# Kernel optimization log

Hardware: AMD Instinct MI355X
Metric: run time of the kernel (lower is better)

The kernel has to match this reference:

```python
import jax, jax.numpy as jnp
import numpy as np

B, T, D = 4, 4096, 2048
K = 1024
H, KVH, HD = 16, 4, 128
FF = 8192
EPS = 1e-6


def _rmsnorm(x, w):
    v = jnp.mean(x * x, axis=-1, keepdims=True)
    return x * jax.lax.rsqrt(v + EPS) * w


def _rotate_half(x):
    x1, x2 = jnp.split(x, 2, axis=-1)
    return jnp.concatenate([-x2, x1], axis=-1)


def setup_inputs() -> dict:
    key = jax.random.key(0)
    ks = jax.random.split(key, 16)
    hidden_states = jax.random.normal(ks[0], (B, T, D), dtype=jnp.float32)
    # unique sorted indices per sequence (top-k selection without duplicates)
    scores = jax.random.uniform(ks[1], (B, T))
    topk_indices = jnp.sort(jax.lax.top_k(scores, K)[1], axis=-1).astype(jnp.int64)
    gating_scores = jax.random.uniform(ks[2], (B, K), dtype=jnp.float32)
    # rotary embeddings over the full sequence [B, T, HD]
    inv = 1.0 / (10000.0 ** (jnp.arange(0, HD, 2, dtype=jnp.float32) / HD))
    ang = jnp.arange(T, dtype=jnp.float32)[:, None] * inv[None, :]  # [T, HD/2]
    emb = jnp.concatenate([ang, ang], axis=-1)
    cos = jnp.broadcast_to(jnp.cos(emb)[None], (B, T, HD)).astype(jnp.float32)
    sin = jnp.broadcast_to(jnp.sin(emb)[None], (B, T, HD)).astype(jnp.float32)
    s = 0.02
    params = dict(
        Wq=jax.random.normal(ks[3], (D, H * HD)) * s,
        bq=jnp.zeros((H * HD,)),
        Wk=jax.random.normal(ks[4], (D, KVH * HD)) * s,
        bk=jnp.zeros((KVH * HD,)),
        Wv=jax.random.normal(ks[5], (D, KVH * HD)) * s,
        bv=jnp.zeros((KVH * HD,)),
        Wo=jax.random.normal(ks[6], (H * HD, D)) * s,
        w_gate=jax.random.normal(ks[7], (D, FF)) * s,
        w_up=jax.random.normal(ks[8], (D, FF)) * s,
        w_down=jax.random.normal(ks[9], (FF, D)) * s,
        ln1_w=jnp.ones((D,)),
        ln2_w=jnp.ones((D,)),
    )
    return dict(hidden_states=hidden_states, topk_indices=topk_indices,
                gating_scores=gating_scores, cos=cos, sin=sin, **params)


def _decoder_layer(x, cos_s, sin_s, Wq, bq, Wk, bk, Wv, bv, Wo,
                   w_gate, w_up, w_down, ln1_w, ln2_w):
    # x: [B, K, D]; cos_s/sin_s: [B, K, HD]
    res = x
    h = _rmsnorm(x, ln1_w)
    q = (h @ Wq + bq).reshape(B, K, H, HD)
    k = (h @ Wk + bk).reshape(B, K, KVH, HD)
    v = (h @ Wv + bv).reshape(B, K, KVH, HD)
    c = cos_s[:, :, None, :]
    s = sin_s[:, :, None, :]
    q = q * c + _rotate_half(q) * s
    k = k * c + _rotate_half(k) * s
    # GQA: repeat kv heads
    k = jnp.repeat(k, H // KVH, axis=2)
    v = jnp.repeat(v, H // KVH, axis=2)
    scores = jnp.einsum('bqhd,bkhd->bhqk', q, k) / np.sqrt(HD)
    causal = jnp.tril(jnp.ones((K, K), dtype=bool))
    scores = jnp.where(causal[None, None], scores, jnp.finfo(scores.dtype).min)
    attn = jax.nn.softmax(scores, axis=-1)
    out = jnp.einsum('bhqk,bkhd->bqhd', attn, v).reshape(B, K, H * HD)
    x = res + out @ Wo
    # MLP (SwiGLU)
    res = x
    h = _rmsnorm(x, ln2_w)
    x = res + (jax.nn.silu(h @ w_gate) * (h @ w_up)) @ w_down
    return x


def reference(hidden_states, topk_indices, gating_scores, cos, sin,
              Wq, bq, Wk, bk, Wv, bv, Wo, w_gate, w_up, w_down, ln1_w, ln2_w):
    idx = topk_indices[:, :, None]  # [B, K, 1]
    selected = jnp.take_along_axis(hidden_states, idx, axis=1)  # [B, K, D]
    cos_s = jnp.take_along_axis(cos, idx, axis=1)
    sin_s = jnp.take_along_axis(sin, idx, axis=1)
    processed = _decoder_layer(selected, cos_s, sin_s, Wq, bq, Wk, bk, Wv, bv,
                               Wo, w_gate, w_up, w_down, ln1_w, ln2_w)
    # soft gating: selected + gate * (processed - selected)
    updated = selected + (processed - selected) * gating_scores[:, :, None]
    b_idx = jnp.arange(B)[:, None]
    final = hidden_states.at[b_idx, topk_indices].set(updated)
    return final
```

## Files before the change

kernel.cpp:

```cpp
#include <hip/hip_runtime.h>
#include <stdint.h>

typedef __bf16 bf16;
typedef __attribute__((ext_vector_type(8))) __bf16 bf16x8;
typedef __attribute__((ext_vector_type(4))) float f32x4;

namespace {

constexpr int cB = 4, cT = 4096, cD = 2048, cK = 1024, cH = 16, cKVH = 4, cHD = 128, cFF = 8192;
constexpr int cM = cB * cK;
constexpr int QKVW = cH * cHD + 2 * cKVH * cHD;

__device__ __forceinline__ void load_lds16(const void* g, void* l) {
  __builtin_amdgcn_global_load_lds((const __attribute__((address_space(1))) void*)g,
                                   (__attribute__((address_space(3))) void*)l, 16, 0, 0);
}

template <int N>
__device__ __forceinline__ void waitcnt_vm() {
  if constexpr (N == 0) asm volatile("s_waitcnt vmcnt(0)" ::: "memory");
  else if constexpr (N == 2) asm volatile("s_waitcnt vmcnt(2)" ::: "memory");
  else if constexpr (N == 3) asm volatile("s_waitcnt vmcnt(3)" ::: "memory");
  else if constexpr (N == 4) asm volatile("s_waitcnt vmcnt(4)" ::: "memory");
  else if constexpr (N == 6) asm volatile("s_waitcnt vmcnt(6)" ::: "memory");
  else if constexpr (N == 8) asm volatile("s_waitcnt vmcnt(8)" ::: "memory");
  else static_assert(N == 0, "unsupported vmcnt literal");
}

template <int OP>
__device__ __forceinline__ float blk_reduce(float v) {
  __shared__ float sm[5];
  const int tid = threadIdx.x, lane = tid & 63, wid = tid >> 6;
#pragma unroll
  for (int o = 32; o; o >>= 1) {
    float o2 = __shfl_down(v, o, 64);
    v = OP ? fmaxf(v, o2) : v + o2;
  }
  if (lane == 0) sm[wid] = v;
  __syncthreads();
  if (tid == 0) {
    float r = sm[0];
#pragma unroll
    for (int i = 1; i < 4; ++i) r = OP ? fmaxf(r, sm[i]) : r + sm[i];
    sm[4] = r;
  }
  __syncthreads();
  float r = sm[4];
  __syncthreads();
  return r;
}

template <int BN, int WM, int WN, int RING, int UNROLL, class Epi>
__global__ __launch_bounds__(512, 2)
void gemm256(const bf16* __restrict__ A, int lda,
             const bf16* __restrict__ Bm, int ldb,
             int Kd, int GM, Epi epi) {
  constexpr int BM = 256;
  constexpr int FM = BM / WM / 16;
  constexpr int FN = BN / WN / 16;
  constexpr int ACALLS = 2;
  constexpr int BCALLS = BN / 128;
  constexpr int L = ACALLS + BCALLS;
  constexpr int D = RING - 1;
  constexpr int SLOTA = BM * 64;
  constexpr int SLOTB = BN * 64;
  constexpr int SLOT = SLOTA + SLOTB;
  __shared__ __align__(16) char lds[RING * SLOT];

  const int tid = threadIdx.x;
  const int lane = tid & 63;
  const int wid = tid >> 6;
  const int l15 = lane & 15, lq = lane >> 4;
  const int wr = wid / WN, wc = wid % WN;

  const int nwg = gridDim.x;
  const int xcd = blockIdx.x & 7, loc = blockIdx.x >> 3;
  const int wg = xcd * (nwg >> 3) + loc;
  const int GN = nwg / GM;
  const int per = 8 * GN;
  const int g = wg / per, r = wg % per;
  const int bm = g * 8 + (r & 7);
  const int bn = r >> 3;

  const bf16* Abase = A + (int64_t)bm * BM * lda;
  const bf16* Bbase = Bm + (int64_t)bn * BN * ldb;

  const bf16* srcA[ACALLS];
  int dstA[ACALLS];
#pragma unroll
  for (int c2 = 0; c2 < ACALLS; ++c2) {
    const int chunk = c2 * 512 + tid;
    const int row = chunk >> 2, pc = chunk & 3;
    const int lc = pc ^ ((row >> 1) & 3);
    srcA[c2] = Abase + (int64_t)row * lda + lc * 8;
    dstA[c2] = chunk * 16;
  }
  const bf16* srcB[BCALLS];
  int dstB[BCALLS];
#pragma unroll
  for (int c2 = 0; c2 < BCALLS; ++c2) {
    const int chunk = c2 * 512 + tid;
    const int row = chunk >> 2, pc = chunk & 3;
    const int lc = pc ^ ((row >> 1) & 3);
    srcB[c2] = Bbase + (int64_t)row * ldb + lc * 8;
    dstB[c2] = chunk * 16;
  }

  int offA[FM], offB[FN];
#pragma unroll
  for (int m = 0; m < FM; ++m) {
    const int row = wr * (BM / WM) + m * 16 + l15;
    offA[m] = row * 64 + (lq ^ ((row >> 1) & 3)) * 16;
  }
#pragma unroll
  for (int n = 0; n < FN; ++n) {
    const int row = wc * (BN / WN) + n * 16 + l15;
    offB[n] = SLOTA + row * 64 + (lq ^ ((row >> 1) & 3)) * 16;
  }

  const int KT = Kd >> 5;
  auto stage = [&](int t) {
    char* sb = lds + (size_t)(t % RING) * SLOT;
#pragma unroll
    for (int c2 = 0; c2 < ACALLS; ++c2)
      load_lds16(srcA[c2] + t * 32, sb + dstA[c2]);
#pragma unroll
    for (int c2 = 0; c2 < BCALLS; ++c2)
      load_lds16(srcB[c2] + t * 32, sb + SLOTA + dstB[c2]);
  };
  auto compute = [&](int t, f32x4 (&acc)[FM][FN]) {
    const char* sb = lds + (size_t)(t % RING) * SLOT;
    bf16x8 av[FM], bv[FN];
#pragma unroll
    for (int m = 0; m < FM; ++m) av[m] = *(const bf16x8*)(sb + offA[m]);
#pragma unroll
    for (int n = 0; n < FN; ++n) bv[n] = *(const bf16x8*)(sb + offB[n]);
    __builtin_amdgcn_s_setprio(1);
#pragma unroll
    for (int m = 0; m < FM; ++m)
#pragma unroll
      for (int n = 0; n < FN; ++n)
        acc[m][n] = __builtin_amdgcn_mfma_f32_16x16x32_bf16(av[m], bv[n], acc[m][n], 0, 0, 0);
    __builtin_amdgcn_s_setprio(0);
  };

  f32x4 acc[FM][FN] = {};

  if constexpr (UNROLL == 1) {
#pragma unroll
    for (int i = 0; i < D; ++i) stage(i);
    waitcnt_vm<(D - 1) * L>();
    __builtin_amdgcn_s_barrier();
    __builtin_amdgcn_sched_barrier(0);
    for (int t = 0; t < KT - D; ++t) {
      stage(t + D);
      compute(t, acc);
      waitcnt_vm<(D - 1) * L>();
      __builtin_amdgcn_s_barrier();
      __builtin_amdgcn_sched_barrier(0);
    }
    waitcnt_vm<0>();
    __builtin_amdgcn_s_barrier();
    for (int t = KT - D; t < KT; ++t) compute(t, acc);
  } else {
    static_assert(RING == 5 && UNROLL == 2, "pair mode is RING=5");
#pragma unroll
    for (int i = 0; i < 3; ++i) stage(i);
    waitcnt_vm<L>();
    __builtin_amdgcn_s_barrier();
    __builtin_amdgcn_sched_barrier(0);
    int t = 0;
    for (; t <= KT - 6; t += 2) {
      stage(t + 3);
      stage(t + 4);
      compute(t, acc);
      compute(t + 1, acc);
      waitcnt_vm<L>();
      __builtin_amdgcn_s_barrier();
      __builtin_amdgcn_sched_barrier(0);
    }
    stage(KT - 1);
    waitcnt_vm<0>();
    __builtin_amdgcn_s_barrier();
    compute(KT - 4, acc);
    compute(KT - 3, acc);
    compute(KT - 2, acc);
    compute(KT - 1, acc);
  }

#pragma unroll
  for (int m = 0; m < FM; ++m) {
    const int r0 = bm * BM + wr * (BM / WM) + m * 16 + lq * 4;
#pragma unroll
    for (int n = 0; n < FN; ++n) {
      const int c1 = bn * BN + wc * (BN / WN) + n * 16 + l15;
#pragma unroll
      for (int j = 0; j < 4; ++j) epi(r0 + j, c1, acc[m][n][j]);
    }
  }
}

__global__ __launch_bounds__(512, 2)
void gemm_gateup8(const bf16* __restrict__ A, const bf16* __restrict__ Bgu,
                  bf16* __restrict__ act) {
  constexpr int QSZ = 64 * 128;
  __shared__ __align__(16) char lds[2 * 8 * QSZ];

  const int tid = threadIdx.x, lane = tid & 63;
  const int wid = tid >> 6;
  const int l15 = lane & 15, lq = lane >> 4;
  const int wr = wid >> 2, wc = wid & 3;

  const int nwg = gridDim.x;
  const int xcd = blockIdx.x & 7, loc = blockIdx.x >> 3;
  const int wg = xcd * (nwg >> 3) + loc;
  const int GM = 16, GN = nwg / GM;
  const int per = 8 * GN;
  const int g = wg / per, r = wg % per;
  const int bm = g * 8 + (r & 7);
  const int bn = r >> 3;

  const bf16* Abase = A + (int64_t)bm * 256 * cD;
  const bf16* Bbase = Bgu + (int64_t)bn * 256 * cD;

  const int srow = tid >> 3, spc = tid & 7;
  const int slc = spc ^ (srow & 7);
  const int sdst = tid * 16;
  const bf16* qsrc[8];
#pragma unroll
  for (int q = 0; q < 4; ++q) qsrc[q] = Abase + (int64_t)(q * 64 + srow) * cD + slc * 8;
#pragma unroll
  for (int q = 0; q < 4; ++q) qsrc[4 + q] = Bbase + (int64_t)(q * 64 + srow) * cD + slc * 8;

  auto stageQ = [&](int buf, int q, int kt) {
    load_lds16(qsrc[q] + kt * 64, lds + (size_t)(buf * 8 + q) * QSZ + sdst);
  };

  f32x4 acc[8][4] = {};
  bf16x8 af[4][2], bfr[2][2];

  auto ldA = [&](int buf, int qr) {
    const char* qb = lds + (size_t)(buf * 8 + wr * 2 + qr) * QSZ;
#pragma unroll
    for (int mq = 0; mq < 4; ++mq) {
      const int rr = mq * 16 + l15;
#pragma unroll
      for (int ks = 0; ks < 2; ++ks)
        af[mq][ks] = *(const bf16x8*)(qb + rr * 128 + (((ks * 4 + lq) ^ (rr & 7)) * 16));
    }
  };
  auto ldB = [&](int buf, int qc) {
    const char* qb = lds + (size_t)(buf * 8 + 4 + wc) * QSZ;
#pragma unroll
    for (int nq = 0; nq < 2; ++nq) {
      const int rr = qc * 32 + nq * 16 + l15;
#pragma unroll
      for (int ks = 0; ks < 2; ++ks)
        bfr[nq][ks] = *(const bf16x8*)(qb + rr * 128 + (((ks * 4 + lq) ^ (rr & 7)) * 16));
    }
  };
  auto mfma16 = [&](int qr, int qc) {
    __builtin_amdgcn_s_setprio(1);
#pragma unroll
    for (int ks = 0; ks < 2; ++ks)
#pragma unroll
      for (int mq = 0; mq < 4; ++mq)
#pragma unroll
        for (int nq = 0; nq < 2; ++nq)
          acc[qr * 4 + mq][qc * 2 + nq] = __builtin_amdgcn_mfma_f32_16x16x32_bf16(
              af[mq][ks], bfr[nq][ks], acc[qr * 4 + mq][qc * 2 + nq], 0, 0, 0);
    __builtin_amdgcn_s_setprio(0);
  };

  const int KT = cD >> 6;

  stageQ(0, 4, 0); stageQ(0, 5, 0);
  stageQ(0, 6, 0); stageQ(0, 7, 0);
  stageQ(0, 0, 0); stageQ(0, 2, 0);
  stageQ(0, 1, 0); stageQ(0, 3, 0);
  waitcnt_vm<2>();
  __builtin_amdgcn_s_barrier();

  for (int t = 0; t < KT; ++t) {
    const int buf = t & 1, nb = buf ^ 1;
    const bool more = (t + 1 < KT);
    ldA(buf, 0);
    ldB(buf, 0);
    if (more) { stageQ(nb, 4, t + 1); stageQ(nb, 5, t + 1); }
    __builtin_amdgcn_s_barrier();
    mfma16(0, 0);
    __builtin_amdgcn_s_barrier();
    ldB(buf, 1);
    if (more) { stageQ(nb, 6, t + 1); stageQ(nb, 7, t + 1); }
    __builtin_amdgcn_s_barrier();
    mfma16(0, 1);
    if (more) waitcnt_vm<4>();
    else      waitcnt_vm<0>();
    __builtin_amdgcn_s_barrier();
    ldA(buf, 1);
    if (more) { stageQ(nb, 0, t + 1); stageQ(nb, 2, t + 1); }
    __builtin_amdgcn_s_barrier();
    mfma16(1, 1);
    __builtin_amdgcn_s_barrier();
    ldB(buf, 0);
    if (more) { stageQ(nb, 1, t + 1); stageQ(nb, 3, t + 1); }
    __builtin_amdgcn_s_barrier();
    mfma16(1, 0);
    if (more) waitcnt_vm<2>();
    __builtin_amdgcn_s_barrier();
  }

#pragma unroll
  for (int m = 0; m < 8; ++m) {
    const int row = bm * 256 + wr * 128 + (m >> 2) * 64 + (m & 3) * 16 + lq * 4;
#pragma unroll
    for (int p = 0; p < 2; ++p) {
      const int col = bn * 128 + wc * 32 + p * 16 + l15;
#pragma unroll
      for (int j = 0; j < 4; ++j) {
        float gv = acc[m][2 * p][j];
        float s = gv / (1.f + __expf(-gv));
        act[(int64_t)(row + j) * cFF + col] = (bf16)(s * acc[m][2 * p + 1][j]);
      }
    }
  }
}

struct EpiQKV {
  bf16* out; const float* bias;
  __device__ void operator()(int r, int c, float v) const {
    out[(int64_t)r * QKVW + c] = (bf16)(v + bias[c]);
  }
};
struct EpiOProj {
  float* x; const float* hidden; const int* topk;
  __device__ void operator()(int r, int c, float v) const {
    int b = r >> 10;
    int t = topk[r];
    x[(int64_t)r * cD + c] = v + hidden[((int64_t)b * cT + t) * cD + c];
  }
};
struct EpiDown {
  float* out; const float* x; const float* hidden; const int* topk; const float* gating;
  __device__ void operator()(int r, int c, float v) const {
    int b = r >> 10;
    int t = topk[r];
    float x2 = v + x[(int64_t)r * cD + c];
    int64_t ho = ((int64_t)b * cT + t) * cD + c;
    float sel = hidden[ho];
    out[ho] = sel + (x2 - sel) * gating[r];
  }
};

__global__ __launch_bounds__(256, 2) void flash_attn(const bf16* __restrict__ qkv,
                                                     const bf16* __restrict__ vt,
                                                     bf16* __restrict__ outb) {
  constexpr int QB = 64, KVB = 128;
  __shared__ __align__(16) char lds[81920];
  char* sK = lds;
  char* sP = lds + 32768;
  char* sV = lds + 49152;

  const int xcdid = blockIdx.x & 7, locid = blockIdx.x >> 3;
  const int wg = xcdid * 128 + locid;
  const int qt = wg & 15, h = (wg >> 4) & 15, b = wg >> 8;
  const int kvh = h >> 2;
  const int qlo = qt * QB;
  const int tid = threadIdx.x, lane = tid & 63, wid = tid >> 6;
  const int l15 = lane & 15, lq = lane >> 4;
  const int wid16 = wid * 16;

  const bf16* qbase = qkv + (int64_t)(b * cK + qlo) * QKVW + h * cHD;
  const bf16* kbase = qkv + (int64_t)(b * cK) * QKVW + cH * cHD + kvh * cHD;
  const bf16* vtbase = vt + (int64_t)(b * cKVH + kvh) * cHD * cK;

#pragma unroll
  for (int c2 = 0; c2 < 4; ++c2) {
    int chunk = c2 * 256 + tid;
    int row = chunk >> 4, c16 = chunk & 15;
    load_lds16(qbase + (int64_t)row * QKVW + (c16 ^ (row & 15)) * 8, sK + chunk * 16);
  }
  __syncthreads();
  bf16x8 qf[4];
  {
    const int row = wid16 + l15;
#pragma unroll
    for (int kt = 0; kt < 4; ++kt)
      qf[kt] = *(const bf16x8*)(sK + row * 256 + (((kt * 4 + lq) ^ (row & 15)) * 16));
  }
  __syncthreads();

  f32x4 oacc[8] = {};
  float m_run[4], l_run[4];
#pragma unroll
  for (int j = 0; j < 4; ++j) { m_run[j] = -3.0e38f; l_run[j] = 0.f; }

  const int jmax = (qlo + QB - 1) >> 7;
  const float sl2e = 0.08838834764831845f * 1.44269504088896f;

  for (int jj = 0; jj <= jmax; ++jj) {
#pragma unroll
    for (int c2 = 0; c2 < 8; ++c2) {
      int chunk = c2 * 256 + tid;
      int row = chunk >> 4, c16 = chunk & 15;
      int cs = (c16 ^ (row & 15)) * 8;
      load_lds16(kbase + (int64_t)(jj * KVB + row) * QKVW + cs, sK + chunk * 16);
      load_lds16(vtbase + (int64_t)row * cK + jj * KVB + cs, sV + chunk * 16);
    }
    __syncthreads();

    f32x4 sacc[8] = {};
#pragma unroll
    for (int kt = 0; kt < 4; ++kt) {
      bf16x8 bv[8];
#pragma unroll
      for (int n = 0; n < 8; ++n) {
        int rk = n * 16 + l15;
        bv[n] = *(const bf16x8*)(sK + rk * 256 + (((kt * 4 + lq) ^ (rk & 15)) * 16));
      }
#pragma unroll
      for (int n = 0; n < 8; ++n)
        sacc[n] = __builtin_amdgcn_mfma_f32_16x16x32_bf16(qf[kt], bv[n], sacc[n], 0, 0, 0);
    }

    if (jj == jmax) {
#pragma unroll
      for (int n = 0; n < 8; ++n)
#pragma unroll
        for (int j = 0; j < 4; ++j) {
          int qrow = qlo + wid16 + lq * 4 + j;
          int kcol = jj * KVB + n * 16 + l15;
          if (kcol > qrow) sacc[n][j] = -3.0e38f;
        }
    }

#pragma unroll
    for (int j = 0; j < 4; ++j) {
      float mx = sacc[0][j];
#pragma unroll
      for (int n = 1; n < 8; ++n) mx = fmaxf(mx, sacc[n][j]);
#pragma unroll
      for (int off = 1; off < 16; off <<= 1) mx = fmaxf(mx, __shfl_xor(mx, off, 64));
      float mnew = fmaxf(m_run[j], mx);
      float corr = exp2f((m_run[j] - mnew) * sl2e);
      m_run[j] = mnew;
      float ps = 0.f;
#pragma unroll
      for (int n = 0; n < 8; ++n) {
        float p = exp2f((sacc[n][j] - mnew) * sl2e);
        sacc[n][j] = p;
        ps += p;
      }
#pragma unroll
      for (int off = 1; off < 16; off <<= 1) ps += __shfl_xor(ps, off, 64);
      l_run[j] = l_run[j] * corr + ps;
#pragma unroll
      for (int n = 0; n < 8; ++n) oacc[n][j] *= corr;
    }

#pragma unroll
    for (int n = 0; n < 8; ++n)
#pragma unroll
      for (int j = 0; j < 4; ++j) {
        int row = wid16 + lq * 4 + j;
        int col = n * 16 + l15;
        int c16 = (col >> 3) ^ (row & 15);
        *(bf16*)(sP + row * 256 + c16 * 16 + (col & 7) * 2) = (bf16)sacc[n][j];
      }
    __syncthreads();

#pragma unroll
    for (int kt = 0; kt < 4; ++kt) {
      const int prow = wid16 + l15;
      bf16x8 av = *(const bf16x8*)(sP + prow * 256 + (((kt * 4 + lq) ^ (prow & 15)) * 16));
      bf16x8 bv[8];
#pragma unroll
      for (int n = 0; n < 8; ++n) {
        int rd = n * 16 + l15;
        bv[n] = *(const bf16x8*)(sV + rd * 256 + (((kt * 4 + lq) ^ (rd & 15)) * 16));
      }
#pragma unroll
      for (int n = 0; n < 8; ++n)
        oacc[n] = __builtin_amdgcn_mfma_f32_16x16x32_bf16(av, bv[n], oacc[n], 0, 0, 0);
    }
    __syncthreads();
  }

#pragma unroll
  for (int j = 0; j < 4; ++j) {
    int row = qlo + wid16 + lq * 4 + j;
    float inv = 1.f / l_run[j];
#pragma unroll
    for (int n = 0; n < 8; ++n) {
      int col = h * cHD + n * 16 + l15;
      outb[((int64_t)b * cK + row) * cD + col] = (bf16)(oacc[n][j] * inv);
    }
  }
}

__global__ void copy_skip(const float4* __restrict__ s, float4* __restrict__ d,
                          const unsigned char* __restrict__ flags, int64_t n) {
  int64_t i = (int64_t)blockIdx.x * blockDim.x + threadIdx.x;
  const int64_t st = (int64_t)gridDim.x * blockDim.x;
  for (; i < n; i += st) {
    int row = (int)(i >> 9);
    if (!flags[row]) d[i] = s[i];
  }
}

__global__ void build_flags(const int* __restrict__ topk, unsigned char* __restrict__ flags) {
  int r = blockIdx.x * 256 + threadIdx.x;
  if (r < cM) flags[(r >> 10) * cT + topk[r]] = 1;
}

__global__ void wconv(const float* __restrict__ src, bf16* __restrict__ dst,
                      int R, int C, int coff, int ldd) {
  __shared__ float t[32][33];
  const int c0 = blockIdx.x * 32, r0 = blockIdx.y * 32;
  for (int rr = threadIdx.y; rr < 32; rr += 8)
    t[rr][threadIdx.x] = src[(int64_t)(r0 + rr) * C + c0 + threadIdx.x];
  __syncthreads();
  for (int rr = threadIdx.y; rr < 32; rr += 8)
    dst[(int64_t)(c0 + rr + coff) * ldd + r0 + threadIdx.x] = (bf16)t[threadIdx.x][rr];
}

__global__ void wconv_gu(const float* __restrict__ srcG, const float* __restrict__ srcU,
                         bf16* __restrict__ dst) {
  __shared__ float t[32][33];
  const float* src = blockIdx.z ? srcU : srcG;
  const int c0 = blockIdx.x * 32, r0 = blockIdx.y * 32;
  for (int rr = threadIdx.y; rr < 32; rr += 8)
    t[rr][threadIdx.x] = src[(int64_t)(r0 + rr) * cFF + c0 + threadIdx.x];
  __syncthreads();
  for (int rr = threadIdx.y; rr < 32; rr += 8) {
    int c = c0 + rr;
    int dr = ((c & ~15) << 1) | (blockIdx.z ? 16 : 0) | (c & 15);
    dst[(int64_t)dr * cD + r0 + threadIdx.x] = (bf16)t[threadIdx.x][rr];
  }
}

__global__ void biascat(const float* __restrict__ bq, const float* __restrict__ bk,
                        const float* __restrict__ bv, float* __restrict__ o) {
  int i = blockIdx.x * 256 + threadIdx.x;
  if (i < QKVW) o[i] = (i < 2048) ? bq[i] : (i < 2560 ? bk[i - 2048] : bv[i - 2560]);
}

__global__ void rmsnorm_rows(const float* __restrict__ base, const int* __restrict__ topk,
                             const float* __restrict__ w, bf16* __restrict__ out) {
  const int r = blockIdx.x;
  const float* src;
  if (topk) {
    int t = topk[r];
    src = base + ((int64_t)(r >> 10) * cT + t) * cD;
  } else {
    src = base + (int64_t)r * cD;
  }
  const int tid = threadIdx.x;
  const float4* s4 = (const float4*)src;
  float4 a = s4[tid * 2], b = s4[tid * 2 + 1];
  float ss = a.x * a.x + a.y * a.y + a.z * a.z + a.w * a.w +
             b.x * b.x + b.y * b.y + b.z * b.z + b.w * b.w;
  float tot = blk_reduce<0>(ss);
  float sc = rsqrtf(tot * (1.f / cD) + 1e-6f);
  bf16* o = out + (int64_t)r * cD;
  const int d0 = tid * 8;
  o[d0 + 0] = (bf16)(a.x * sc * w[d0 + 0]);
  o[d0 + 1] = (bf16)(a.y * sc * w[d0 + 1]);
  o[d0 + 2] = (bf16)(a.z * sc * w[d0 + 2]);
  o[d0 + 3] = (bf16)(a.w * sc * w[d0 + 3]);
  o[d0 + 4] = (bf16)(b.x * sc * w[d0 + 4]);
  o[d0 + 5] = (bf16)(b.y * sc * w[d0 + 5]);
  o[d0 + 6] = (bf16)(b.z * sc * w[d0 + 6]);
  o[d0 + 7] = (bf16)(b.w * sc * w[d0 + 7]);
}

__global__ void rope_kernel(bf16* __restrict__ qkv, const float* __restrict__ cosb,
                            const float* __restrict__ sinb, const int* __restrict__ topk) {
  const int r = blockIdx.x;
  const int b = r >> 10;
  const int t = topk[r];
  const float* cr = cosb + ((int64_t)b * cT + t) * cHD;
  const float* sr = sinb + ((int64_t)b * cT + t) * cHD;
  bf16* rowq = qkv + (int64_t)r * QKVW;
  for (int p = threadIdx.x; p < (cH + cKVH) * 64; p += 256) {
    int hh = p >> 6, d = p & 63;
    bf16* base = (hh < cH) ? (rowq + hh * cHD) : (rowq + cH * cHD + (hh - cH) * cHD);
    float x1 = (float)base[d], x2 = (float)base[d + 64];
    float c1 = cr[d], s1 = sr[d], c2 = cr[d + 64], s2 = sr[d + 64];
    base[d] = (bf16)(x1 * c1 - x2 * s1);
    base[d + 64] = (bf16)(x2 * c2 + x1 * s2);
  }
}

__global__ void vtrans(const bf16* __restrict__ qkv, bf16* __restrict__ Vt) {
  __shared__ bf16 t[32][33];
  const int bz = blockIdx.z, b = bz >> 2, kv = bz & 3;
  const int k0 = blockIdx.x * 32, d0 = blockIdx.y * 32;
  for (int rr = threadIdx.y; rr < 32; rr += 8)
    t[rr][threadIdx.x] =
        qkv[(int64_t)(b * cK + k0 + rr) * QKVW + cH * cHD + cKVH * cHD + kv * cHD + d0 + threadIdx.x];
  __syncthreads();
  for (int rr = threadIdx.y; rr < 32; rr += 8)
    Vt[((int64_t)(b * cKVH + kv) * cHD + d0 + rr) * cK + k0 + threadIdx.x] = t[threadIdx.x][rr];
}

}

extern "C" void kernel_launch(void* const* d_in, const int* in_sizes, int n_in,
                              void* d_out, int out_size, void* d_ws, size_t ws_size,
                              hipStream_t stream) {
  const float* hidden = (const float*)d_in[0];
  const int* topk = (const int*)d_in[1];
  const float* gating = (const float*)d_in[2];
  const float* cosb = (const float*)d_in[3];
  const float* sinb = (const float*)d_in[4];
  const float* Wq = (const float*)d_in[5];
  const float* bq = (const float*)d_in[6];
  const float* Wk = (const float*)d_in[7];
  const float* bk = (const float*)d_in[8];
  const float* Wv = (const float*)d_in[9];
  const float* bv = (const float*)d_in[10];
  const float* Wo = (const float*)d_in[11];
  const float* wg = (const float*)d_in[12];
  const float* wu = (const float*)d_in[13];
  const float* wd = (const float*)d_in[14];
  const float* ln1 = (const float*)d_in[15];
  const float* ln2 = (const float*)d_in[16];
  float* out = (float*)d_out;
  (void)in_sizes; (void)n_in; (void)out_size; (void)ws_size;

  char* ws = (char*)d_ws;
  size_t off = 0;
  auto alloc = [&](size_t bytes) {
    char* p = ws + off;
    off += (bytes + 255) & ~(size_t)255;
    return p;
  };
  bf16* wt_qkv = (bf16*)alloc((size_t)QKVW * cD * 2);
  bf16* wt_o = (bf16*)alloc((size_t)cD * cD * 2);
  bf16* wt_gu = (bf16*)alloc((size_t)2 * cFF * cD * 2);
  bf16* wt_d = (bf16*)alloc((size_t)cD * cFF * 2);
  float* bias_cat = (float*)alloc((size_t)QKVW * 4);
  bf16* hbuf = (bf16*)alloc((size_t)cM * cD * 2);
  bf16* qkv = (bf16*)alloc((size_t)cM * QKVW * 2);
  bf16* vt = (bf16*)alloc((size_t)cB * cKVH * cHD * cK * 2);
  bf16* attnout = (bf16*)alloc((size_t)cM * cD * 2);
  float* xbuf = (float*)alloc((size_t)cM * cD * 4);
  bf16* actbuf = (bf16*)alloc((size_t)cM * cFF * 2);
  unsigned char* flags = (unsigned char*)alloc((size_t)cB * cT);

  (void)hipMemsetAsync(flags, 0, (size_t)cB * cT, stream);
  build_flags<<<cM / 256, 256, 0, stream>>>(topk, flags);
  copy_skip<<<2048, 256, 0, stream>>>((const float4*)hidden, (float4*)out, flags,
                                      (int64_t)cB * cT * cD / 4);

  const dim3 tb(32, 8);
  wconv<<<dim3(cD / 32, cD / 32), tb, 0, stream>>>(Wq, wt_qkv, cD, cD, 0, cD);
  wconv<<<dim3(512 / 32, cD / 32), tb, 0, stream>>>(Wk, wt_qkv, cD, 512, 2048, cD);
  wconv<<<dim3(512 / 32, cD / 32), tb, 0, stream>>>(Wv, wt_qkv, cD, 512, 2560, cD);
  wconv<<<dim3(cD / 32, cD / 32), tb, 0, stream>>>(Wo, wt_o, cD, cD, 0, cD);
  wconv_gu<<<dim3(cFF / 32, cD / 32, 2), tb, 0, stream>>>(wg, wu, wt_gu);
  wconv<<<dim3(cD / 32, cFF / 32), tb, 0, stream>>>(wd, wt_d, cFF, cD, 0, cFF);
  biascat<<<(QKVW + 255) / 256, 256, 0, stream>>>(bq, bk, bv, bias_cat);

  rmsnorm_rows<<<cM, 256, 0, stream>>>(hidden, topk, ln1, hbuf);
  gemm256<256, 2, 4, 5, 2, EpiQKV><<<16 * (QKVW / 256), 512, 0, stream>>>(
      hbuf, cD, wt_qkv, cD, cD, 16, EpiQKV{qkv, bias_cat});
  rope_kernel<<<cM, 256, 0, stream>>>(qkv, cosb, sinb, topk);
  vtrans<<<dim3(cK / 32, cHD / 32, cB * cKVH), tb, 0, stream>>>(qkv, vt);

  flash_attn<<<1024, 256, 0, stream>>>(qkv, vt, attnout);

  gemm256<128, 4, 2, 5, 2, EpiOProj><<<16 * (cD / 128), 512, 0, stream>>>(
      attnout, cD, wt_o, cD, cD, 16, EpiOProj{xbuf, hidden, topk});
  rmsnorm_rows<<<cM, 256, 0, stream>>>(xbuf, nullptr, ln2, hbuf);
  gemm_gateup8<<<16 * (2 * cFF / 256), 512, 0, stream>>>(hbuf, wt_gu, actbuf);
  gemm256<128, 4, 2, 5, 2, EpiDown><<<16 * (cD / 128), 512, 0, stream>>>(
      actbuf, cFF, wt_d, cFF, cFF, 16, EpiDown{out, xbuf, hidden, topk, gating});
}
```

Baseline: 835.8 us.

## Shrink gate/up GEMM tile to 256x128 with K=32 steps for higher occupancy

The fused gate/up SwiGLU GEMM now uses a 256x128 output tile (interleaved gate/up columns) instead of 256x256, and a K-step of 32 instead of 64. This cuts LDS use to 48KB and accumulators to 16 per wave, so launch bounds can request 4 blocks per CU and twice as many workgroups are launched. The aim is better latency hiding through occupancy. The cost is lower arithmetic intensity per tile, twice as many K iterations with barriers, and more global traffic for A.

```diff
diff --git a/kernel.cpp b/kernel.cpp
--- a/kernel.cpp
+++ b/kernel.cpp
@@ -19,6 +19,7 @@
 template <int N>
 __device__ __forceinline__ void waitcnt_vm() {
   if constexpr (N == 0) asm volatile("s_waitcnt vmcnt(0)" ::: "memory");
+  else if constexpr (N == 1) asm volatile("s_waitcnt vmcnt(1)" ::: "memory");
   else if constexpr (N == 2) asm volatile("s_waitcnt vmcnt(2)" ::: "memory");
   else if constexpr (N == 3) asm volatile("s_waitcnt vmcnt(3)" ::: "memory");
   else if constexpr (N == 4) asm volatile("s_waitcnt vmcnt(4)" ::: "memory");
@@ -200,11 +201,11 @@
   }
 }
 
-__global__ __launch_bounds__(512, 2)
-void gemm_gateup8(const bf16* __restrict__ A, const bf16* __restrict__ Bgu,
+__global__ __launch_bounds__(512, 4)
+void gemm_gateup9(const bf16* __restrict__ A, const bf16* __restrict__ Bgu,
                   bf16* __restrict__ act) {
-  constexpr int QSZ = 64 * 128;
-  __shared__ __align__(16) char lds[2 * 8 * QSZ];
+  constexpr int QSZ = 64 * 64;
+  __shared__ __align__(16) char lds[2 * 6 * QSZ];
 
   const int tid = threadIdx.x, lane = tid & 63;
   const int wid = tid >> 6;
@@ -221,107 +222,94 @@
   const int bn = r >> 3;
 
   const bf16* Abase = A + (int64_t)bm * 256 * cD;
-  const bf16* Bbase = Bgu + (int64_t)bn * 256 * cD;
-
-  const int srow = tid >> 3, spc = tid & 7;
-  const int slc = spc ^ (srow & 7);
-  const int sdst = tid * 16;
-  const bf16* qsrc[8];
-#pragma unroll
-  for (int q = 0; q < 4; ++q) qsrc[q] = Abase + (int64_t)(q * 64 + srow) * cD + slc * 8;
-#pragma unroll
-  for (int q = 0; q < 4; ++q) qsrc[4 + q] = Bbase + (int64_t)(q * 64 + srow) * cD + slc * 8;
-
-  auto stageQ = [&](int buf, int q, int kt) {
-    load_lds16(qsrc[q] + kt * 64, lds + (size_t)(buf * 8 + q) * QSZ + sdst);
+  const bf16* Bbase = Bgu + (int64_t)bn * 128 * cD;
+
+  const int sub = tid >> 8, cc = tid & 255;
+  const int srow = cc >> 2, spc = cc & 3;
+  const int slc = spc ^ ((srow >> 1) & 3);
+  const bf16* psrc[3];
+  int pdst[3];
+  {
+    const int qB = sub;
+    psrc[0] = Bbase + (int64_t)(qB * 64 + srow) * cD + slc * 8;
+    pdst[0] = (4 + qB) * QSZ + cc * 16;
+    const int qA0 = sub * 2;
+    psrc[1] = Abase + (int64_t)(qA0 * 64 + srow) * cD + slc * 8;
+    pdst[1] = qA0 * QSZ + cc * 16;
+    const int qA1 = 1 + sub * 2;
+    psrc[2] = Abase + (int64_t)(qA1 * 64 + srow) * cD + slc * 8;
+    pdst[2] = qA1 * QSZ + cc * 16;
+  }
+  auto stageP = [&](int buf, int p, int kt) {
+    load_lds16(psrc[p] + kt * 32, lds + (size_t)buf * 6 * QSZ + pdst[p]);
   };
 
-  f32x4 acc[8][4] = {};
-  bf16x8 af[4][2], bfr[2][2];
-
-  auto ldA = [&](int buf, int qr) {
-    const char* qb = lds + (size_t)(buf * 8 + wr * 2 + qr) * QSZ;
+  f32x4 acc[8][2] = {};
+  bf16x8 af[4], bfr[2];
+
+  auto ldA = [&](int buf, int half) {
+    const char* qb = lds + (size_t)(buf * 6 + wr * 2 + half) * QSZ;
 #pragma unroll
     for (int mq = 0; mq < 4; ++mq) {
       const int rr = mq * 16 + l15;
-#pragma unroll
-      for (int ks = 0; ks < 2; ++ks)
-        af[mq][ks] = *(const bf16x8*)(qb + rr * 128 + (((ks * 4 + lq) ^ (rr & 7)) * 16));
+      af[mq] = *(const bf16x8*)(qb + rr * 64 + ((lq ^ ((rr >> 1) & 3)) * 16));
     }
   };
-  auto ldB = [&](int buf, int qc) {
-    const char* qb = lds + (size_t)(buf * 8 + 4 + wc) * QSZ;
+  auto ldB = [&](int buf) {
+    const char* qb = lds + (size_t)(buf * 6 + 4 + (wc >> 1)) * QSZ;
 #pragma unroll
     for (int nq = 0; nq < 2; ++nq) {
-      const int rr = qc * 32 + nq * 16 + l15;
-#pragma unroll
-      for (int ks = 0; ks < 2; ++ks)
-        bfr[nq][ks] = *(const bf16x8*)(qb + rr * 128 + (((ks * 4 + lq) ^ (rr & 7)) * 16));
+      const int rr = (wc & 1) * 32 + nq * 16 + l15;
+      bfr[nq] = *(const bf16x8*)(qb + rr * 64 + ((lq ^ ((rr >> 1) & 3)) * 16));
     }
   };
-  auto mfma16 = [&](int qr, int qc) {
+  auto mfma8 = [&](int half) {
     __builtin_amdgcn_s_setprio(1);
 #pragma unroll
-    for (int ks = 0; ks < 2; ++ks)
-#pragma unroll
-      for (int mq = 0; mq < 4; ++mq)
-#pragma unroll
-        for (int nq = 0; nq < 2; ++nq)
-          acc[qr * 4 + mq][qc * 2 + nq] = __builtin_amdgcn_mfma_f32_16x16x32_bf16(
-              af[mq][ks], bfr[nq][ks], acc[qr * 4 + mq][qc * 2 + nq], 0, 0, 0);
+    for (int mq = 0; mq < 4; ++mq)
+#pragma unroll
+      for (int nq = 0; nq < 2; ++nq)
+        acc[half * 4 + mq][nq] = __builtin_amdgcn_mfma_f32_16x16x32_bf16(
+            af[mq], bfr[nq], acc[half * 4 + mq][nq], 0, 0, 0);
     __builtin_amdgcn_s_setprio(0);
   };
 
-  const int KT = cD >> 6;
-
-  stageQ(0, 4, 0); stageQ(0, 5, 0);
-  stageQ(0, 6, 0); stageQ(0, 7, 0);
-  stageQ(0, 0, 0); stageQ(0, 2, 0);
-  stageQ(0, 1, 0); stageQ(0, 3, 0);
-  waitcnt_vm<2>();
+  const int KT = cD >> 5;
+
+  stageP(0, 0, 0);
+  stageP(0, 1, 0);
+  stageP(0, 2, 0);
+  waitcnt_vm<1>();
   __builtin_amdgcn_s_barrier();
 
   for (int t = 0; t < KT; ++t) {
     const int buf = t & 1, nb = buf ^ 1;
     const bool more = (t + 1 < KT);
+    ldB(buf);
     ldA(buf, 0);
-    ldB(buf, 0);
-    if (more) { stageQ(nb, 4, t + 1); stageQ(nb, 5, t + 1); }
-    __builtin_amdgcn_s_barrier();
-    mfma16(0, 0);
-    __builtin_amdgcn_s_barrier();
-    ldB(buf, 1);
-    if (more) { stageQ(nb, 6, t + 1); stageQ(nb, 7, t + 1); }
-    __builtin_amdgcn_s_barrier();
-    mfma16(0, 1);
-    if (more) waitcnt_vm<4>();
+    if (more) { stageP(nb, 0, t + 1); stageP(nb, 1, t + 1); }
+    __builtin_amdgcn_s_barrier();
+    mfma8(0);
+    if (more) waitcnt_vm<2>();
     else      waitcnt_vm<0>();
     __builtin_amdgcn_s_barrier();
     ldA(buf, 1);
-    if (more) { stageQ(nb, 0, t + 1); stageQ(nb, 2, t + 1); }
-    __builtin_amdgcn_s_barrier();
-    mfma16(1, 1);
-    __builtin_amdgcn_s_barrier();
-    ldB(buf, 0);
-    if (more) { stageQ(nb, 1, t + 1); stageQ(nb, 3, t + 1); }
-    __builtin_amdgcn_s_barrier();
-    mfma16(1, 0);
-    if (more) waitcnt_vm<2>();
+    if (more) stageP(nb, 2, t + 1);
+    __builtin_amdgcn_s_barrier();
+    mfma8(1);
+    if (more) waitcnt_vm<1>();
     __builtin_amdgcn_s_barrier();
   }
 
 #pragma unroll
   for (int m = 0; m < 8; ++m) {
-    const int row = bm * 256 + wr * 128 + (m >> 2) * 64 + (m & 3) * 16 + lq * 4;
-#pragma unroll
-    for (int p = 0; p < 2; ++p) {
-      const int col = bn * 128 + wc * 32 + p * 16 + l15;
-#pragma unroll
-      for (int j = 0; j < 4; ++j) {
-        float gv = acc[m][2 * p][j];
-        float s = gv / (1.f + __expf(-gv));
-        act[(int64_t)(row + j) * cFF + col] = (bf16)(s * acc[m][2 * p + 1][j]);
-      }
+    const int row = bm * 256 + wr * 128 + m * 16 + lq * 4;
+    const int col = bn * 64 + wc * 16 + l15;
+#pragma unroll
+    for (int j = 0; j < 4; ++j) {
+      float gv = acc[m][0][j];
+      float s = gv / (1.f + __expf(-gv));
+      act[(int64_t)(row + j) * cFF + col] = (bf16)(s * acc[m][1][j]);
     }
   }
 }
@@ -674,7 +662,7 @@
   gemm256<128, 4, 2, 5, 2, EpiOProj><<<16 * (cD / 128), 512, 0, stream>>>(
       attnout, cD, wt_o, cD, cD, 16, EpiOProj{xbuf, hidden, topk});
   rmsnorm_rows<<<cM, 256, 0, stream>>>(xbuf, nullptr, ln2, hbuf);
-  gemm_gateup8<<<16 * (2 * cFF / 256), 512, 0, stream>>>(hbuf, wt_gu, actbuf);
+  gemm_gateup9<<<16 * (2 * cFF / 128), 512, 0, stream>>>(hbuf, wt_gu, actbuf);
   gemm256<128, 4, 2, 5, 2, EpiDown><<<16 * (cD / 128), 512, 0, stream>>>(
       actbuf, cFF, wt_d, cFF, cFF, 16, EpiDown{out, xbuf, hidden, topk, gating});
 }
```

Measured after the change: 888.0 us. 6.2% more time.
